# Optimization experiments

Hardware: AMD Instinct MI355X
Metric: run time of the kernel (lower is better)

Reference implementation:

```python
import jax, jax.numpy as jnp
import numpy as np

NUM_EDGE_CLASS = 4
NODE_DIM = 64
BATCH = 32
NUM_NODES = 1024


def setup_inputs() -> dict:
    key = jax.random.key(0)
    k1, k2, k3, k4, k5 = jax.random.split(key, 5)
    node_state = jax.random.normal(k1, (BATCH, NUM_NODES, NODE_DIM), dtype=jnp.float32)
    adj_mat = jax.random.randint(k2, (BATCH, NUM_NODES, NUM_NODES), 0, NUM_EDGE_CLASS, dtype=jnp.int32)
    matrix_in = jax.random.normal(k3, (NUM_EDGE_CLASS, NODE_DIM, NODE_DIM), dtype=jnp.float32) * 0.1
    matrix_out = jax.random.normal(k4, (NUM_EDGE_CLASS, NODE_DIM, NODE_DIM), dtype=jnp.float32) * 0.1
    bias = jax.random.normal(k5, (2 * NODE_DIM,), dtype=jnp.float32)
    return {"node_state": node_state, "adj_mat": adj_mat,
            "matrix_in": matrix_in, "matrix_out": matrix_out, "bias": bias}


def reference(node_state, adj_mat, matrix_in, matrix_out, bias):
    """GGNN message passing (Li et al. Eq. 2).

    Original TF code builds a [b, n*d, n*d] block matrix where block (i, j)
    is matrix_in[adj_mat[b, i, j]] (and matrix_out[adj_mat[b, j, i]] for the
    outgoing direction), then matmuls against flattened node states. The
    equivalent fused math is:
      m_in[b,i]  = sum_j matrix_in[adj[b,i,j]]  @ h[b,j]
      m_out[b,i] = sum_j matrix_out[adj[b,j,i]] @ h[b,j]
    Implemented via a one-hot over the (small) set of edge classes so the
    per-edge d x d matrices are never materialized per edge.
    """
    h = node_state  # [b, n, d]
    onehot = jax.nn.one_hot(adj_mat, NUM_EDGE_CLASS, dtype=h.dtype)  # [b, n, n, c]
    # per-class neighbor aggregation, then one small matmul per class
    s_in = jnp.einsum('bijc,bje->bice', onehot, h)          # [b, n, c, d]
    m_in = jnp.einsum('bice,cde->bid', s_in, matrix_in)      # [b, n, d]
    s_out = jnp.einsum('bjic,bje->bice', onehot, h)          # transposed adjacency
    m_out = jnp.einsum('bice,cde->bid', s_out, matrix_out)   # [b, n, d]
    message = jnp.concatenate([m_in, m_out], axis=-1) + bias  # [b, n, 2d]
    return message
```

## Files before the change

kernel.cpp:

```cpp
#include <hip/hip_runtime.h>


namespace {

typedef unsigned int  u32;
typedef unsigned short u16;
typedef __attribute__((ext_vector_type(8))) short bf16x8;
typedef __attribute__((ext_vector_type(4))) float f32x4;

constexpr int NN = 1024;
constexpr int ND = 64;

__device__ inline u16 f2bf(float x) {
    u32 u = __float_as_uint(x);
    return (u16)((u + 0x7FFFu + ((u >> 16) & 1u)) >> 16);
}
__device__ inline float bf2f(u16 x) { return __uint_as_float(((u32)x) << 16); }

#if defined(__has_builtin)
#if __has_builtin(__builtin_amdgcn_global_load_lds)
#define HAVE_GLL 1
#endif
#endif

__device__ inline void async_copy16(const void* g, void* l) {
#ifdef HAVE_GLL
    typedef __attribute__((address_space(1))) const u32 gu32;
    typedef __attribute__((address_space(3))) u32 lu32;
    __builtin_amdgcn_global_load_lds((gu32*)g, (lu32*)l, 16, 0, 0);
#else
    int lane = threadIdx.x & 63;
    ((uint4*)l)[lane] = *(const uint4*)((const char*)g);
#endif
}

__global__ __launch_bounds__(256) void pack_adj(
    const int* __restrict__ adj, u32* __restrict__ adjP, u32* __restrict__ adjPT)
{
    __shared__ u32 rp[64][16];
    const int t = threadIdx.x;
    const int bid = blockIdx.x;
    const int b = bid >> 6, It = (bid >> 4) & 3, Jt = (bid >> 2) & 3, s = bid & 3;
    const int* base = adj + ((size_t)b << 20) + (size_t)(It * 256 + s * 64) * NN + Jt * 256;

    const int row = t >> 2, seg = t & 3;
    const int* rptr = base + (size_t)row * NN + seg * 64;
    u32 w[4];
    #pragma unroll
    for (int q = 0; q < 4; ++q) {
        int4 v0 = *(const int4*)(rptr + q * 16 + 0);
        int4 v1 = *(const int4*)(rptr + q * 16 + 4);
        int4 v2 = *(const int4*)(rptr + q * 16 + 8);
        int4 v3 = *(const int4*)(rptr + q * 16 + 12);
        u32 u = (u32)(v0.x & 3) | ((u32)(v0.y & 3) << 2) | ((u32)(v0.z & 3) << 4) | ((u32)(v0.w & 3) << 6)
              | ((u32)(v1.x & 3) << 8) | ((u32)(v1.y & 3) << 10) | ((u32)(v1.z & 3) << 12) | ((u32)(v1.w & 3) << 14)
              | ((u32)(v2.x & 3) << 16) | ((u32)(v2.y & 3) << 18) | ((u32)(v2.z & 3) << 20) | ((u32)(v2.w & 3) << 22)
              | ((u32)(v3.x & 3) << 24) | ((u32)(v3.y & 3) << 26) | ((u32)(v3.z & 3) << 28) | ((u32)(v3.w & 3) << 30);
        w[q] = u;
    }
    u32* op = adjP + (((((size_t)b * 4 + Jt) * 16 + It * 4 + s) * 4 + seg) * 64 + row) * 4;
    *(uint4*)op = make_uint4(w[0], w[1], w[2], w[3]);
    *(uint4*)&rp[row][seg * 4] = make_uint4(w[0], w[1], w[2], w[3]);
    __syncthreads();

    const int sc = t >> 6, il = t & 63;
    const int cw = sc * 4 + (il >> 4);
    const int bp = (il & 15) * 2;
    u32 o[4];
    #pragma unroll
    for (int jj = 0; jj < 4; ++jj) {
        u32 acc = 0;
        #pragma unroll
        for (int k = 0; k < 16; ++k)
            acc |= ((rp[jj * 16 + k][cw] >> bp) & 3u) << (2 * k);
        o[jj] = acc;
    }
    u32* op2 = adjPT + (((((size_t)b * 4 + It) * 16 + Jt * 4 + sc) * 4 + s) * 64 + il) * 4;
    *(uint4*)op2 = make_uint4(o[0], o[1], o[2], o[3]);
}

__global__ __launch_bounds__(256) void prep_h(
    const float* __restrict__ h, u16* __restrict__ Hws, float* __restrict__ PA)
{
    __shared__ u16 hl[256][72];
    const int t = threadIdx.x;
    const int b = blockIdx.x >> 2, jc = blockIdx.x & 3;
    const float* hb = h + ((size_t)b * NN + jc * 256) * ND;
    #pragma unroll
    for (int k = 0; k < 16; ++k) {
        int j = k * 16 + (t >> 4);
        int e4 = (t & 15) * 4;
        float4 v = *(const float4*)(hb + (size_t)j * ND + e4);
        *(u32*)&hl[j][e4]     = (u32)f2bf(v.x) | ((u32)f2bf(v.y) << 16);
        *(u32*)&hl[j][e4 + 2] = (u32)f2bf(v.z) | ((u32)f2bf(v.w) << 16);
    }
    __syncthreads();
    u16* ob = Hws + (size_t)(b * 4 + jc) * 2048 * 8;
    const int e = t & 63;
    float psum = 0.f;
    #pragma unroll
    for (int k = 0; k < 8; ++k) {
        int u = k * 4 + (t >> 6);
        u32 p0, p1, p2, p3;
        u16 x0 = hl[u * 8 + 0][e], x1 = hl[u * 8 + 1][e], x2 = hl[u * 8 + 2][e], x3 = hl[u * 8 + 3][e];
        u16 x4 = hl[u * 8 + 4][e], x5 = hl[u * 8 + 5][e], x6 = hl[u * 8 + 6][e], x7 = hl[u * 8 + 7][e];
        psum += bf2f(x0) + bf2f(x1) + bf2f(x2) + bf2f(x3) + bf2f(x4) + bf2f(x5) + bf2f(x6) + bf2f(x7);
        p0 = (u32)x0 | ((u32)x1 << 16); p1 = (u32)x2 | ((u32)x3 << 16);
        p2 = (u32)x4 | ((u32)x5 << 16); p3 = (u32)x6 | ((u32)x7 << 16);
        *(uint4*)(ob + (size_t)(u * 64 + e) * 8) = make_uint4(p0, p1, p2, p3);
    }
    atomicAdd(&PA[b * 64 + e], psum);
}

__global__ __launch_bounds__(256) void prep_m(
    const float* __restrict__ Min, const float* __restrict__ Mout,
    const float* __restrict__ bias, const float* __restrict__ PA,
    u16* __restrict__ Mws, float* __restrict__ basews)
{
    const int t = threadIdx.x, bb = blockIdx.x;
    if (bb == 0) {
        for (int i = t; i < 2 * 4096; i += 256) {
            const float* M = (i < 4096) ? Min : Mout;
            int idx = i & 4095;
            float m0 = M[idx], m1 = M[4096 + idx], m2 = M[8192 + idx], m3 = M[12288 + idx];
            u16* o = Mws + (size_t)(i >> 12) * 3 * 4096;
            o[idx]            = f2bf(m1 - m0);
            o[4096 + idx]     = f2bf(m2 - m0);
            o[8192 + idx]     = f2bf(m0 - m1 - m2 + m3);
        }
    }
    if (t < 128) {
        int d = t & 63, dir = t >> 6;
        const float* M0 = (dir ? Mout : Min) + d * 64;
        float s = bias[dir * 64 + d];
        #pragma unroll 8
        for (int e = 0; e < 64; ++e) s += PA[bb * 64 + e] * M0[e];
        basews[(bb * 2 + dir) * 64 + d] = s;
    }
}

__global__ __launch_bounds__(256, 4) void ggnn_main(
    const u32* __restrict__ adjP, const u32* __restrict__ adjPT,
    const u16* __restrict__ Hws, const u16* __restrict__ Mws,
    const float* __restrict__ basews, float* __restrict__ out)
{
    __shared__ __align__(16) char smem[36864];
    char* adjL = smem;
    char* hL   = smem + 4096;
    u16 (*Sb)[16][72] = (u16(*)[16][72])smem;

    const int t = threadIdx.x;
    const int w = t >> 6, lane = t & 63;
    const int ln = t & 15, qd = (t & 63) >> 4, qd2 = qd >> 1;
    const int shamt = (qd & 1) * 16;
    const int bid = blockIdx.x;
    const int dir = bid >> 9;
    const int b = (bid >> 4) & 31, it = bid & 15;

    const u32* Adir = dir ? adjPT : adjP;
    f32x4 acc[3][4];
    #pragma unroll
    for (int p = 0; p < 3; ++p)
        #pragma unroll
        for (int nt = 0; nt < 4; ++nt) acc[p][nt] = (f32x4){0.f, 0.f, 0.f, 0.f};

    for (int jc = 0; jc < 4; ++jc) {
        __syncthreads();
        const char* at = (const char*)(Adir + (size_t)((b * 4 + jc) * 16 + it) * 1024);
        const char* ht = (const char*)(Hws + (size_t)(b * 4 + jc) * 16384);
        if (w == 0) {
            #pragma unroll
            for (int u = 0; u < 4; ++u)
                async_copy16(at + u * 1024 + lane * 16, adjL + u * 1024);
        }
        #pragma unroll
        for (int k = 0; k < 8; ++k) {
            int i = w + k * 4;
            async_copy16(ht + i * 1024 + lane * 16, hL + i * 1024);
        }
        __syncthreads();

        uint4 Ar[4];
        #pragma unroll
        for (int u = 0; u < 4; ++u)
            Ar[u] = *(const uint4*)(adjL + (u * 64 + w * 16 + ln) * 16);

        #pragma unroll
        for (int ks = 0; ks < 8; ++ks) {
            uint4 Q = Ar[ks >> 1];
            u32 a = (ks & 1) ? (qd2 ? Q.w : Q.z) : (qd2 ? Q.y : Q.x);
            u32 f  = (a >> shamt) & 0xFFFFu;
            u32 x0 = f & 0x5555u;
            u32 x1 = (f >> 1) & 0x5555u;
            u32 xt = x0 & x1;
            bf16x8 bf[4];
            #pragma unroll
            for (int nt = 0; nt < 4; ++nt)
                bf[nt] = *(const bf16x8*)(hL + ((ks * 4 + qd) * 64 + nt * 16 + ln) * 16);
            #pragma unroll
            for (int p = 0; p < 3; ++p) {
                u32 xp = (p == 0) ? x0 : (p == 1) ? x1 : xt;
                union { u32 u[4]; bf16x8 v; } A;
                #pragma unroll
                for (int wd = 0; wd < 4; ++wd) {
                    u32 z = xp >> (4 * wd);
                    A.u[wd] = ((z & 1u) | ((z & 4u) << 14)) * 0x3F80u;
                }
                #pragma unroll
                for (int nt = 0; nt < 4; ++nt)
                    acc[p][nt] = __builtin_amdgcn_mfma_f32_16x16x32_bf16(
                        A.v, bf[nt], acc[p][nt], 0, 0, 0);
            }
        }
    }

    __syncthreads();

    #pragma unroll
    for (int p = 0; p < 3; ++p)
        #pragma unroll
        for (int nt = 0; nt < 4; ++nt)
            #pragma unroll
            for (int r = 0; r < 4; ++r)
                Sb[w * 3 + p][qd * 4 + r][nt * 16 + ln] = f2bf(acc[p][nt][r]);

    const float* bv = basews + (b * 2 + dir) * 64;
    f32x4 acc2[4];
    #pragma unroll
    for (int dt = 0; dt < 4; ++dt) {
        float v = bv[dt * 16 + ln];
        acc2[dt] = (f32x4){v, v, v, v};
    }
    const u16* Mb = Mws + (size_t)dir * 3 * 4096;
    #pragma unroll
    for (int p = 0; p < 3; ++p) {
        #pragma unroll
        for (int ks2 = 0; ks2 < 2; ++ks2) {
            bf16x8 af = *(const bf16x8*)&Sb[w * 3 + p][ln][ks2 * 32 + qd * 8];
            #pragma unroll
            for (int dt = 0; dt < 4; ++dt) {
                bf16x8 mf = *(const bf16x8*)(Mb + (size_t)(p * 64 + dt * 16 + ln) * 64
                                             + ks2 * 32 + qd * 8);
                acc2[dt] = __builtin_amdgcn_mfma_f32_16x16x32_bf16(af, mf, acc2[dt], 0, 0, 0);
            }
        }
    }
    #pragma unroll
    for (int dt = 0; dt < 4; ++dt)
        #pragma unroll
        for (int r = 0; r < 4; ++r)
            out[((size_t)b * NN + it * 64 + w * 16 + qd * 4 + r) * 128
                + dir * 64 + dt * 16 + ln] = acc2[dt][r];
}

}

extern "C" void kernel_launch(void* const* d_in, const int* in_sizes, int n_in,
                              void* d_out, int out_size, void* d_ws, size_t ws_size,
                              hipStream_t stream) {
    (void)in_sizes; (void)n_in; (void)out_size; (void)ws_size;
    const float* h    = (const float*)d_in[0];
    const int*   adj  = (const int*)d_in[1];
    const float* Min  = (const float*)d_in[2];
    const float* Mout = (const float*)d_in[3];
    const float* bias = (const float*)d_in[4];
    float* out = (float*)d_out;

    char* ws = (char*)d_ws;
    u32* adjP   = (u32*)(ws + 0);
    u32* adjPT  = (u32*)(ws + 8388608);
    u16* Hws    = (u16*)(ws + 16777216);
    float* PA   = (float*)(ws + 20971520);
    u16* Mws    = (u16*)(ws + 20979712);
    float* basews = (float*)(ws + 21028864);

    hipMemsetAsync(PA, 0, 32 * 64 * sizeof(float), stream);
    pack_adj<<<2048, 256, 0, stream>>>(adj, adjP, adjPT);
    prep_h<<<128, 256, 0, stream>>>(h, Hws, PA);
    prep_m<<<32, 256, 0, stream>>>(Min, Mout, bias, PA, Mws, basews);
    ggnn_main<<<1024, 256, 0, stream>>>(adjP, adjPT, Hws, Mws, basews, out);
}
```

Baseline: 263.9 us.

## Merge prep kernels, compute both directions per block with double-buffered staging

Fuses adjacency packing and h preparation into one launch and replaces the atomic partial-sum with per-block partials reduced in prep_m, which removes the memset and one kernel launch. The main kernel now processes both in and out directions in a single block. Each staged h tile is reused for two adjacency streams, which halves H traffic and the grid size. The block also double-buffers LDS loads so the next chunk's copy overlaps compute. The cost is twice the accumulator registers, 80KB of LDS, and occupancy lowered to 2 blocks per CU.

```diff
diff --git a/kernel.cpp b/kernel.cpp
--- a/kernel.cpp
+++ b/kernel.cpp
@@ -34,90 +34,98 @@
 #endif
 }
 
-__global__ __launch_bounds__(256) void pack_adj(
-    const int* __restrict__ adj, u32* __restrict__ adjP, u32* __restrict__ adjPT)
+__global__ __launch_bounds__(256) void pack_and_preph(
+    const int* __restrict__ adj, u32* __restrict__ adjP, u32* __restrict__ adjPT,
+    const float* __restrict__ h, u16* __restrict__ Hws, float* __restrict__ PApart)
 {
-    __shared__ u32 rp[64][16];
+    __shared__ __align__(16) char sm1[36864];
     const int t = threadIdx.x;
     const int bid = blockIdx.x;
-    const int b = bid >> 6, It = (bid >> 4) & 3, Jt = (bid >> 2) & 3, s = bid & 3;
-    const int* base = adj + ((size_t)b << 20) + (size_t)(It * 256 + s * 64) * NN + Jt * 256;
-
-    const int row = t >> 2, seg = t & 3;
-    const int* rptr = base + (size_t)row * NN + seg * 64;
-    u32 w[4];
-    #pragma unroll
-    for (int q = 0; q < 4; ++q) {
-        int4 v0 = *(const int4*)(rptr + q * 16 + 0);
-        int4 v1 = *(const int4*)(rptr + q * 16 + 4);
-        int4 v2 = *(const int4*)(rptr + q * 16 + 8);
-        int4 v3 = *(const int4*)(rptr + q * 16 + 12);
-        u32 u = (u32)(v0.x & 3) | ((u32)(v0.y & 3) << 2) | ((u32)(v0.z & 3) << 4) | ((u32)(v0.w & 3) << 6)
-              | ((u32)(v1.x & 3) << 8) | ((u32)(v1.y & 3) << 10) | ((u32)(v1.z & 3) << 12) | ((u32)(v1.w & 3) << 14)
-              | ((u32)(v2.x & 3) << 16) | ((u32)(v2.y & 3) << 18) | ((u32)(v2.z & 3) << 20) | ((u32)(v2.w & 3) << 22)
-              | ((u32)(v3.x & 3) << 24) | ((u32)(v3.y & 3) << 26) | ((u32)(v3.z & 3) << 28) | ((u32)(v3.w & 3) << 30);
-        w[q] = u;
-    }
-    u32* op = adjP + (((((size_t)b * 4 + Jt) * 16 + It * 4 + s) * 4 + seg) * 64 + row) * 4;
-    *(uint4*)op = make_uint4(w[0], w[1], w[2], w[3]);
-    *(uint4*)&rp[row][seg * 4] = make_uint4(w[0], w[1], w[2], w[3]);
-    __syncthreads();
-
-    const int sc = t >> 6, il = t & 63;
-    const int cw = sc * 4 + (il >> 4);
-    const int bp = (il & 15) * 2;
-    u32 o[4];
-    #pragma unroll
-    for (int jj = 0; jj < 4; ++jj) {
-        u32 acc = 0;
-        #pragma unroll
-        for (int k = 0; k < 16; ++k)
-            acc |= ((rp[jj * 16 + k][cw] >> bp) & 3u) << (2 * k);
-        o[jj] = acc;
-    }
-    u32* op2 = adjPT + (((((size_t)b * 4 + It) * 16 + Jt * 4 + sc) * 4 + s) * 64 + il) * 4;
-    *(uint4*)op2 = make_uint4(o[0], o[1], o[2], o[3]);
-}
-
-__global__ __launch_bounds__(256) void prep_h(
-    const float* __restrict__ h, u16* __restrict__ Hws, float* __restrict__ PA)
-{
-    __shared__ u16 hl[256][72];
-    const int t = threadIdx.x;
-    const int b = blockIdx.x >> 2, jc = blockIdx.x & 3;
-    const float* hb = h + ((size_t)b * NN + jc * 256) * ND;
-    #pragma unroll
-    for (int k = 0; k < 16; ++k) {
-        int j = k * 16 + (t >> 4);
-        int e4 = (t & 15) * 4;
-        float4 v = *(const float4*)(hb + (size_t)j * ND + e4);
-        *(u32*)&hl[j][e4]     = (u32)f2bf(v.x) | ((u32)f2bf(v.y) << 16);
-        *(u32*)&hl[j][e4 + 2] = (u32)f2bf(v.z) | ((u32)f2bf(v.w) << 16);
-    }
-    __syncthreads();
-    u16* ob = Hws + (size_t)(b * 4 + jc) * 2048 * 8;
-    const int e = t & 63;
-    float psum = 0.f;
-    #pragma unroll
-    for (int k = 0; k < 8; ++k) {
-        int u = k * 4 + (t >> 6);
-        u32 p0, p1, p2, p3;
-        u16 x0 = hl[u * 8 + 0][e], x1 = hl[u * 8 + 1][e], x2 = hl[u * 8 + 2][e], x3 = hl[u * 8 + 3][e];
-        u16 x4 = hl[u * 8 + 4][e], x5 = hl[u * 8 + 5][e], x6 = hl[u * 8 + 6][e], x7 = hl[u * 8 + 7][e];
-        psum += bf2f(x0) + bf2f(x1) + bf2f(x2) + bf2f(x3) + bf2f(x4) + bf2f(x5) + bf2f(x6) + bf2f(x7);
-        p0 = (u32)x0 | ((u32)x1 << 16); p1 = (u32)x2 | ((u32)x3 << 16);
-        p2 = (u32)x4 | ((u32)x5 << 16); p3 = (u32)x6 | ((u32)x7 << 16);
-        *(uint4*)(ob + (size_t)(u * 64 + e) * 8) = make_uint4(p0, p1, p2, p3);
-    }
-    atomicAdd(&PA[b * 64 + e], psum);
+
+    if (bid < 2048) {
+        u32 (*rp)[16] = (u32(*)[16])sm1;
+        const int b = bid >> 6, It = (bid >> 4) & 3, Jt = (bid >> 2) & 3, s = bid & 3;
+        const int* base = adj + ((size_t)b << 20) + (size_t)(It * 256 + s * 64) * NN + Jt * 256;
+
+        const int row = t >> 2, seg = t & 3;
+        const int* rptr = base + (size_t)row * NN + seg * 64;
+        u32 w[4];
+        #pragma unroll
+        for (int q = 0; q < 4; ++q) {
+            int4 v0 = *(const int4*)(rptr + q * 16 + 0);
+            int4 v1 = *(const int4*)(rptr + q * 16 + 4);
+            int4 v2 = *(const int4*)(rptr + q * 16 + 8);
+            int4 v3 = *(const int4*)(rptr + q * 16 + 12);
+            u32 u = (u32)(v0.x & 3) | ((u32)(v0.y & 3) << 2) | ((u32)(v0.z & 3) << 4) | ((u32)(v0.w & 3) << 6)
+                  | ((u32)(v1.x & 3) << 8) | ((u32)(v1.y & 3) << 10) | ((u32)(v1.z & 3) << 12) | ((u32)(v1.w & 3) << 14)
+                  | ((u32)(v2.x & 3) << 16) | ((u32)(v2.y & 3) << 18) | ((u32)(v2.z & 3) << 20) | ((u32)(v2.w & 3) << 22)
+                  | ((u32)(v3.x & 3) << 24) | ((u32)(v3.y & 3) << 26) | ((u32)(v3.z & 3) << 28) | ((u32)(v3.w & 3) << 30);
+            w[q] = u;
+        }
+        u32* op = adjP + (((((size_t)b * 4 + Jt) * 16 + It * 4 + s) * 4 + seg) * 64 + row) * 4;
+        *(uint4*)op = make_uint4(w[0], w[1], w[2], w[3]);
+        *(uint4*)&rp[row][seg * 4] = make_uint4(w[0], w[1], w[2], w[3]);
+        __syncthreads();
+
+        const int sc = t >> 6, il = t & 63;
+        const int cw = sc * 4 + (il >> 4);
+        const int bp = (il & 15) * 2;
+        u32 o[4];
+        #pragma unroll
+        for (int jj = 0; jj < 4; ++jj) {
+            u32 acc = 0;
+            #pragma unroll
+            for (int k = 0; k < 16; ++k)
+                acc |= ((rp[jj * 16 + k][cw] >> bp) & 3u) << (2 * k);
+            o[jj] = acc;
+        }
+        u32* op2 = adjPT + (((((size_t)b * 4 + It) * 16 + Jt * 4 + sc) * 4 + s) * 64 + il) * 4;
+        *(uint4*)op2 = make_uint4(o[0], o[1], o[2], o[3]);
+    } else {
+        u16 (*hl)[72] = (u16(*)[72])sm1;
+        const int pb = bid - 2048;
+        const int b = pb >> 2, jc = pb & 3;
+        const float* hb = h + ((size_t)b * NN + jc * 256) * ND;
+        #pragma unroll
+        for (int k = 0; k < 16; ++k) {
+            int j = k * 16 + (t >> 4);
+            int e4 = (t & 15) * 4;
+            float4 v = *(const float4*)(hb + (size_t)j * ND + e4);
+            *(u32*)&hl[j][e4]     = (u32)f2bf(v.x) | ((u32)f2bf(v.y) << 16);
+            *(u32*)&hl[j][e4 + 2] = (u32)f2bf(v.z) | ((u32)f2bf(v.w) << 16);
+        }
+        __syncthreads();
+        u16* ob = Hws + (size_t)(b * 4 + jc) * 2048 * 8;
+        const int e = t & 63;
+        float psum = 0.f;
+        #pragma unroll
+        for (int k = 0; k < 8; ++k) {
+            int u = k * 4 + (t >> 6);
+            u32 p0, p1, p2, p3;
+            u16 x0 = hl[u * 8 + 0][e], x1 = hl[u * 8 + 1][e], x2 = hl[u * 8 + 2][e], x3 = hl[u * 8 + 3][e];
+            u16 x4 = hl[u * 8 + 4][e], x5 = hl[u * 8 + 5][e], x6 = hl[u * 8 + 6][e], x7 = hl[u * 8 + 7][e];
+            psum += bf2f(x0) + bf2f(x1) + bf2f(x2) + bf2f(x3) + bf2f(x4) + bf2f(x5) + bf2f(x6) + bf2f(x7);
+            p0 = (u32)x0 | ((u32)x1 << 16); p1 = (u32)x2 | ((u32)x3 << 16);
+            p2 = (u32)x4 | ((u32)x5 << 16); p3 = (u32)x6 | ((u32)x7 << 16);
+            *(uint4*)(ob + (size_t)(u * 64 + e) * 8) = make_uint4(p0, p1, p2, p3);
+        }
+        PApart[(size_t)(b * 4 + jc) * 256 + (t >> 6) * 64 + e] = psum;
+    }
 }
 
 __global__ __launch_bounds__(256) void prep_m(
     const float* __restrict__ Min, const float* __restrict__ Mout,
-    const float* __restrict__ bias, const float* __restrict__ PA,
+    const float* __restrict__ bias, const float* __restrict__ PApart,
     u16* __restrict__ Mws, float* __restrict__ basews)
 {
+    __shared__ float PAb[64];
     const int t = threadIdx.x, bb = blockIdx.x;
+    if (t < 64) {
+        float s = 0.f;
+        #pragma unroll
+        for (int q = 0; q < 16; ++q) s += PApart[(size_t)bb * 1024 + q * 64 + t];
+        PAb[t] = s;
+    }
     if (bb == 0) {
         for (int i = t; i < 2 * 4096; i += 256) {
             const float* M = (i < 4096) ? Min : Mout;
@@ -129,24 +137,23 @@
             o[8192 + idx]     = f2bf(m0 - m1 - m2 + m3);
         }
     }
+    __syncthreads();
     if (t < 128) {
         int d = t & 63, dir = t >> 6;
         const float* M0 = (dir ? Mout : Min) + d * 64;
         float s = bias[dir * 64 + d];
         #pragma unroll 8
-        for (int e = 0; e < 64; ++e) s += PA[bb * 64 + e] * M0[e];
+        for (int e = 0; e < 64; ++e) s += PAb[e] * M0[e];
         basews[(bb * 2 + dir) * 64 + d] = s;
     }
 }
 
-__global__ __launch_bounds__(256, 4) void ggnn_main(
+__global__ __launch_bounds__(256, 2) void ggnn_main(
     const u32* __restrict__ adjP, const u32* __restrict__ adjPT,
     const u16* __restrict__ Hws, const u16* __restrict__ Mws,
     const float* __restrict__ basews, float* __restrict__ out)
 {
-    __shared__ __align__(16) char smem[36864];
-    char* adjL = smem;
-    char* hL   = smem + 4096;
+    __shared__ __align__(16) char smem[81920];
     u16 (*Sb)[16][72] = (u16(*)[16][72])smem;
 
     const int t = threadIdx.x;
@@ -154,103 +161,124 @@
     const int ln = t & 15, qd = (t & 63) >> 4, qd2 = qd >> 1;
     const int shamt = (qd & 1) * 16;
     const int bid = blockIdx.x;
-    const int dir = bid >> 9;
-    const int b = (bid >> 4) & 31, it = bid & 15;
-
-    const u32* Adir = dir ? adjPT : adjP;
-    f32x4 acc[3][4];
+    const int b = bid >> 4, it = bid & 15;
+
+    f32x4 acc[2][3][4];
     #pragma unroll
-    for (int p = 0; p < 3; ++p)
-        #pragma unroll
-        for (int nt = 0; nt < 4; ++nt) acc[p][nt] = (f32x4){0.f, 0.f, 0.f, 0.f};
-
+    for (int d = 0; d < 2; ++d)
+        #pragma unroll
+        for (int p = 0; p < 3; ++p)
+            #pragma unroll
+            for (int nt = 0; nt < 4; ++nt) acc[d][p][nt] = (f32x4){0.f, 0.f, 0.f, 0.f};
+
+    auto stage = [&](int buf, int jc) {
+        char* hL = smem + buf * 32768;
+        char* aL = smem + 65536 + buf * 8192;
+        const char* ht = (const char*)(Hws + (size_t)(b * 4 + jc) * 16384);
+        #pragma unroll
+        for (int k = 0; k < 8; ++k) {
+            int i = k * 4 + w;
+            async_copy16(ht + i * 1024 + lane * 16, hL + i * 1024);
+        }
+        if (w < 2) {
+            const u32* Ad = w ? adjPT : adjP;
+            const char* at = (const char*)(Ad + (size_t)((b * 4 + jc) * 16 + it) * 1024);
+            #pragma unroll
+            for (int u = 0; u < 4; ++u)
+                async_copy16(at + u * 1024 + lane * 16, aL + w * 4096 + u * 1024);
+        }
+    };
+
+    stage(0, 0);
+    __syncthreads();
+
+    int buf = 0;
     for (int jc = 0; jc < 4; ++jc) {
-        __syncthreads();
-        const char* at = (const char*)(Adir + (size_t)((b * 4 + jc) * 16 + it) * 1024);
-        const char* ht = (const char*)(Hws + (size_t)(b * 4 + jc) * 16384);
-        if (w == 0) {
+        if (jc < 3) stage(buf ^ 1, jc + 1);
+
+        const char* hL = smem + buf * 32768;
+        const char* aL = smem + 65536 + buf * 8192;
+        uint4 Ar[2][4];
+        #pragma unroll
+        for (int d = 0; d < 2; ++d)
             #pragma unroll
             for (int u = 0; u < 4; ++u)
-                async_copy16(at + u * 1024 + lane * 16, adjL + u * 1024);
-        }
-        #pragma unroll
-        for (int k = 0; k < 8; ++k) {
-            int i = w + k * 4;
-            async_copy16(ht + i * 1024 + lane * 16, hL + i * 1024);
-        }
-        __syncthreads();
-
-        uint4 Ar[4];
-        #pragma unroll
-        for (int u = 0; u < 4; ++u)
-            Ar[u] = *(const uint4*)(adjL + (u * 64 + w * 16 + ln) * 16);
+                Ar[d][u] = *(const uint4*)(aL + d * 4096 + (u * 64 + w * 16 + ln) * 16);
 
         #pragma unroll
         for (int ks = 0; ks < 8; ++ks) {
-            uint4 Q = Ar[ks >> 1];
-            u32 a = (ks & 1) ? (qd2 ? Q.w : Q.z) : (qd2 ? Q.y : Q.x);
-            u32 f  = (a >> shamt) & 0xFFFFu;
-            u32 x0 = f & 0x5555u;
-            u32 x1 = (f >> 1) & 0x5555u;
-            u32 xt = x0 & x1;
             bf16x8 bf[4];
             #pragma unroll
             for (int nt = 0; nt < 4; ++nt)
                 bf[nt] = *(const bf16x8*)(hL + ((ks * 4 + qd) * 64 + nt * 16 + ln) * 16);
             #pragma unroll
-            for (int p = 0; p < 3; ++p) {
-                u32 xp = (p == 0) ? x0 : (p == 1) ? x1 : xt;
-                union { u32 u[4]; bf16x8 v; } A;
+            for (int d = 0; d < 2; ++d) {
+                uint4 Q = Ar[d][ks >> 1];
+                u32 a = (ks & 1) ? (qd2 ? Q.w : Q.z) : (qd2 ? Q.y : Q.x);
+                u32 f  = (a >> shamt) & 0xFFFFu;
+                u32 x0 = f & 0x5555u;
+                u32 x1 = (f >> 1) & 0x5555u;
+                u32 xt = x0 & x1;
                 #pragma unroll
-                for (int wd = 0; wd < 4; ++wd) {
-                    u32 z = xp >> (4 * wd);
-                    A.u[wd] = ((z & 1u) | ((z & 4u) << 14)) * 0x3F80u;
+                for (int p = 0; p < 3; ++p) {
+                    u32 xp = (p == 0) ? x0 : (p == 1) ? x1 : xt;
+                    union { u32 u[4]; bf16x8 v; } A;
+                    #pragma unroll
+                    for (int wd = 0; wd < 4; ++wd) {
+                        u32 z = xp >> (4 * wd);
+                        A.u[wd] = ((z & 1u) | ((z & 4u) << 14)) * 0x3F80u;
+                    }
+                    #pragma unroll
+                    for (int nt = 0; nt < 4; ++nt)
+                        acc[d][p][nt] = __builtin_amdgcn_mfma_f32_16x16x32_bf16(
+                            A.v, bf[nt], acc[d][p][nt], 0, 0, 0);
                 }
+            }
+        }
+        __syncthreads();
+        buf ^= 1;
+    }
+
+    #pragma unroll
+    for (int d = 0; d < 2; ++d)
+        #pragma unroll
+        for (int p = 0; p < 3; ++p)
+            #pragma unroll
+            for (int nt = 0; nt < 4; ++nt)
                 #pragma unroll
-                for (int nt = 0; nt < 4; ++nt)
-                    acc[p][nt] = __builtin_amdgcn_mfma_f32_16x16x32_bf16(
-                        A.v, bf[nt], acc[p][nt], 0, 0, 0);
+                for (int r = 0; r < 4; ++r)
+                    Sb[(w * 2 + d) * 3 + p][qd * 4 + r][nt * 16 + ln] = f2bf(acc[d][p][nt][r]);
+
+    #pragma unroll
+    for (int d = 0; d < 2; ++d) {
+        const float* bv = basews + (b * 2 + d) * 64;
+        f32x4 acc2[4];
+        #pragma unroll
+        for (int dt = 0; dt < 4; ++dt) {
+            float v = bv[dt * 16 + ln];
+            acc2[dt] = (f32x4){v, v, v, v};
+        }
+        const u16* Mb = Mws + (size_t)d * 3 * 4096;
+        #pragma unroll
+        for (int p = 0; p < 3; ++p) {
+            #pragma unroll
+            for (int ks2 = 0; ks2 < 2; ++ks2) {
+                bf16x8 af = *(const bf16x8*)&Sb[(w * 2 + d) * 3 + p][ln][ks2 * 32 + qd * 8];
+                #pragma unroll
+                for (int dt = 0; dt < 4; ++dt) {
+                    bf16x8 mf = *(const bf16x8*)(Mb + (size_t)(p * 64 + dt * 16 + ln) * 64
+                                                 + ks2 * 32 + qd * 8);
+                    acc2[dt] = __builtin_amdgcn_mfma_f32_16x16x32_bf16(af, mf, acc2[dt], 0, 0, 0);
+                }
             }
         }
-    }
-
-    __syncthreads();
-
-    #pragma unroll
-    for (int p = 0; p < 3; ++p)
-        #pragma unroll
-        for (int nt = 0; nt < 4; ++nt)
+        #pragma unroll
+        for (int dt = 0; dt < 4; ++dt)
             #pragma unroll
             for (int r = 0; r < 4; ++r)
-                Sb[w * 3 + p][qd * 4 + r][nt * 16 + ln] = f2bf(acc[p][nt][r]);
-
-    const float* bv = basews + (b * 2 + dir) * 64;
-    f32x4 acc2[4];
-    #pragma unroll
-    for (int dt = 0; dt < 4; ++dt) {
-        float v = bv[dt * 16 + ln];
-        acc2[dt] = (f32x4){v, v, v, v};
-    }
-    const u16* Mb = Mws + (size_t)dir * 3 * 4096;
-    #pragma unroll
-    for (int p = 0; p < 3; ++p) {
-        #pragma unroll
-        for (int ks2 = 0; ks2 < 2; ++ks2) {
-            bf16x8 af = *(const bf16x8*)&Sb[w * 3 + p][ln][ks2 * 32 + qd * 8];
-            #pragma unroll
-            for (int dt = 0; dt < 4; ++dt) {
-                bf16x8 mf = *(const bf16x8*)(Mb + (size_t)(p * 64 + dt * 16 + ln) * 64
-                                             + ks2 * 32 + qd * 8);
-                acc2[dt] = __builtin_amdgcn_mfma_f32_16x16x32_bf16(af, mf, acc2[dt], 0, 0, 0);
-            }
-        }
-    }
-    #pragma unroll
-    for (int dt = 0; dt < 4; ++dt)
-        #pragma unroll
-        for (int r = 0; r < 4; ++r)
-            out[((size_t)b * NN + it * 64 + w * 16 + qd * 4 + r) * 128
-                + dir * 64 + dt * 16 + ln] = acc2[dt][r];
+                out[((size_t)b * NN + it * 64 + w * 16 + qd * 4 + r) * 128
+                    + d * 64 + dt * 16 + ln] = acc2[dt][r];
+    }
 }
 
 }
@@ -267,16 +295,14 @@
     float* out = (float*)d_out;
 
     char* ws = (char*)d_ws;
-    u32* adjP   = (u32*)(ws + 0);
-    u32* adjPT  = (u32*)(ws + 8388608);
-    u16* Hws    = (u16*)(ws + 16777216);
-    float* PA   = (float*)(ws + 20971520);
-    u16* Mws    = (u16*)(ws + 20979712);
-    float* basews = (float*)(ws + 21028864);
-
-    hipMemsetAsync(PA, 0, 32 * 64 * sizeof(float), stream);
-    pack_adj<<<2048, 256, 0, stream>>>(adj, adjP, adjPT);
-    prep_h<<<128, 256, 0, stream>>>(h, Hws, PA);
-    prep_m<<<32, 256, 0, stream>>>(Min, Mout, bias, PA, Mws, basews);
-    ggnn_main<<<1024, 256, 0, stream>>>(adjP, adjPT, Hws, Mws, basews, out);
-}
+    u32* adjP     = (u32*)(ws + 0);
+    u32* adjPT    = (u32*)(ws + 8388608);
+    u16* Hws      = (u16*)(ws + 16777216);
+    float* PApart = (float*)(ws + 20971520);
+    u16* Mws      = (u16*)(ws + 21102592);
+    float* basews = (float*)(ws + 21151744);
+
+    pack_and_preph<<<2176, 256, 0, stream>>>(adj, adjP, adjPT, h, Hws, PApart);
+    prep_m<<<32, 256, 0, stream>>>(Min, Mout, bias, PApart, Mws, basews);
+    ggnn_main<<<512, 256, 0, stream>>>(adjP, adjPT, Hws, Mws, basews, out);
+}
```

After: 259.5 us. No clear change (-1.7%).
